# Kernel tuning notes

Measured on AMD Instinct MI355X. Metric: run time of the kernel, lower is better.

The kernel has to match this reference:

```python
import jax, jax.numpy as jnp
import numpy as np

E, D, H = 8, 512, 2048  # num_experts, features, features*mlp_ratio
B, S = 4, 512


def _lecun(key, shape):
    fan_in = shape[-2] if len(shape) >= 2 else shape[0]
    return jax.random.normal(key, shape, dtype=jnp.float32) / jnp.sqrt(jnp.float32(fan_in))


def setup_inputs() -> dict:
    key = jax.random.key(0)
    ks = jax.random.split(key, 8)
    return {
        'x_real': jax.random.normal(ks[0], (B, S, D), dtype=jnp.float32),
        'x_imag': jax.random.normal(ks[1], (B, S, D), dtype=jnp.float32),
        # gating Dense over concat([amp, phase]) -> in_features = 2*D
        'gate_W': _lecun(ks[2], (2 * D, E)),
        'gate_b': jnp.zeros((E,), jnp.float32),
        # per-expert ComplexLinear 1: D -> H
        'W1r': _lecun(ks[3], (E, D, H)),
        'W1i': _lecun(ks[4], (E, D, H)),
        'b1r': jnp.zeros((E, H), jnp.float32),
        'b1i': jnp.zeros((E, H), jnp.float32),
        # per-expert ComplexModReLU bias
        'mod_b': jnp.zeros((E, H), jnp.float32),
        # per-expert ComplexLinear 2: H -> D
        'W2r': _lecun(ks[5], (E, H, D)),
        'W2i': _lecun(ks[6], (E, H, D)),
        'b2r': jnp.zeros((E, D), jnp.float32),
        'b2i': jnp.zeros((E, D), jnp.float32),
    }


def reference(x_real, x_imag, gate_W, gate_b, W1r, W1i, b1r, b1i, mod_b, W2r, W2i, b2r, b2i):
    eps = 1e-10
    # --- gating: scores over [|z|, angle(z)] ---
    amp = jnp.sqrt(x_real ** 2 + x_imag ** 2)            # |z|, [B,S,D]
    phase = jnp.arctan2(x_imag, x_real)                  # angle(z)
    routing_input = jnp.concatenate([amp, phase], axis=-1)  # [B,S,2D]
    scores = routing_input @ gate_W + gate_b             # [B,S,E]
    probs = jax.nn.softmax(scores, axis=-1)
    idx = jnp.argmax(probs, axis=-1)                     # [B,S] top-1 expert

    # --- all experts dense (faithful to reference): complex linear 1 ---
    # (Wr + iWi)(xr + ixi) : hr = xr Wr - xi Wi ; hi = xr Wi + xi Wr
    h_r = (jnp.einsum('bsd,edh->ebsh', x_real, W1r)
           - jnp.einsum('bsd,edh->ebsh', x_imag, W1i)) + b1r[:, None, None, :]
    h_i = (jnp.einsum('bsd,edh->ebsh', x_real, W1i)
           + jnp.einsum('bsd,edh->ebsh', x_imag, W1r)) + b1i[:, None, None, :]

    # --- ComplexModReLU: relu(|z|+b) * z / (|z|+eps), |z| = sqrt(r^2+i^2+eps) ---
    a = jnp.sqrt(h_r ** 2 + h_i ** 2 + eps)              # [E,B,S,H]
    scale = jax.nn.relu(a + mod_b[:, None, None, :]) / (a + eps)
    h_r = h_r * scale
    h_i = h_i * scale

    # --- complex linear 2 ---
    o_r = (jnp.einsum('ebsh,ehd->ebsd', h_r, W2r)
           - jnp.einsum('ebsh,ehd->ebsd', h_i, W2i)) + b2r[:, None, None, :]
    o_i = (jnp.einsum('ebsh,ehd->ebsd', h_r, W2i)
           + jnp.einsum('ebsh,ehd->ebsd', h_i, W2r)) + b2i[:, None, None, :]

    # --- mask + weight (top-1): out = sum_e out_e * probs[...,e] * (argmax==e) ---
    e_ids = jnp.arange(probs.shape[-1])
    w = jnp.transpose(probs, (2, 0, 1)) * (idx[None, :, :] == e_ids[:, None, None])  # [E,B,S]
    out_r = jnp.einsum('ebs,ebsd->bsd', w, o_r)
    out_i = jnp.einsum('ebs,ebsd->bsd', w, o_i)
    return (out_r, out_i)
```

## Files before the change

### kernel.cpp

```cpp
#include <hip/hip_runtime.h>
#include <math.h>

#define NE 8
#define ND 512
#define NH 2048
#define NT 2048

typedef __attribute__((ext_vector_type(8)))  short short8;
typedef __attribute__((ext_vector_type(16))) float f32x16;

#define GLL(g, d) __builtin_amdgcn_global_load_lds( \
    (const __attribute__((address_space(1))) void*)(g), \
    (__attribute__((address_space(3))) void*)(d), 16, 0, 0)

__device__ __forceinline__ unsigned short f2bf(float x) {
    unsigned int u = __builtin_bit_cast(unsigned int, x);
    u += 0x7FFFu + ((u >> 16) & 1u);
    return (unsigned short)(u >> 16);
}

__device__ __forceinline__ short8 neg8(short8 v) {
    int4 u = __builtin_bit_cast(int4, v);
    u.x ^= 0x80008000; u.y ^= 0x80008000; u.z ^= 0x80008000; u.w ^= 0x80008000;
    return __builtin_bit_cast(short8, u);
}

__device__ __forceinline__ short8 lds8(const unsigned short* p) {
    return *(const short8*)p;
}

__global__ __launch_bounds__(256) void gate_kernel(
    const float* __restrict__ xr, const float* __restrict__ xi,
    const float* __restrict__ gW, const float* __restrict__ gb,
    float* __restrict__ gate_w,
    int* __restrict__ counts, int* __restrict__ tok_list,
    unsigned short* __restrict__ xbr, unsigned short* __restrict__ xbi)
{
    int t = blockIdx.x;
    int tid = threadIdx.x;
    const float* xrt = xr + (size_t)t * ND;
    const float* xit = xi + (size_t)t * ND;
    unsigned short* obr = xbr + (size_t)t * ND;
    unsigned short* obi = xbi + (size_t)t * ND;

    float acc[NE] = {0,0,0,0,0,0,0,0};
    for (int r = tid; r < 2 * ND; r += 256) {
        int d = r & (ND - 1);
        float a = xrt[d], b = xit[d];
        float v;
        if (r < ND) {
            v = sqrtf(a * a + b * b);
            obr[d] = f2bf(a);
            obi[d] = f2bf(b);
        } else {
            v = atan2f(b, a);
        }
        const float4* g = (const float4*)(gW + (size_t)r * NE);
        float4 g0 = g[0], g1 = g[1];
        acc[0] += v * g0.x; acc[1] += v * g0.y; acc[2] += v * g0.z; acc[3] += v * g0.w;
        acc[4] += v * g1.x; acc[5] += v * g1.y; acc[6] += v * g1.z; acc[7] += v * g1.w;
    }
    #pragma unroll
    for (int e = 0; e < NE; e++) {
        for (int off = 32; off > 0; off >>= 1)
            acc[e] += __shfl_down(acc[e], off, 64);
    }
    __shared__ float part[4][NE];
    int wave = tid >> 6, lane = tid & 63;
    if (lane == 0) {
        #pragma unroll
        for (int e = 0; e < NE; e++) part[wave][e] = acc[e];
    }
    __syncthreads();
    if (tid == 0) {
        float s[NE];
        #pragma unroll
        for (int e = 0; e < NE; e++)
            s[e] = part[0][e] + part[1][e] + part[2][e] + part[3][e] + gb[e];
        int amax = 0; float m = s[0];
        #pragma unroll
        for (int e = 1; e < NE; e++) if (s[e] > m) { m = s[e]; amax = e; }
        float denom = 0.f;
        #pragma unroll
        for (int e = 0; e < NE; e++) denom += expf(s[e] - m);
        gate_w[t] = 1.0f / denom;
        int pos = atomicAdd(&counts[amax], 1);
        tok_list[amax * NT + pos] = t;
    }
}

__global__ __launch_bounds__(256) void transw_kernel(
    const float* __restrict__ s0, unsigned short* __restrict__ d0,
    const float* __restrict__ s1, unsigned short* __restrict__ d1,
    int R, int C)
{
    __shared__ unsigned int tile[64 * 33];
    int e = blockIdx.z;
    int c0 = blockIdx.x * 64, r0 = blockIdx.y * 64;
    size_t off = (size_t)e * R * C;
    int tid = threadIdx.x;
    int rl = tid >> 4;
    int c4 = (tid & 15) * 4;
    int r4 = (tid & 15) * 4;
    #pragma unroll
    for (int p = 0; p < 2; ++p) {
        const float* src = (p ? s1 : s0) + off;
        unsigned short* dst = (p ? d1 : d0) + off;
        if (p) __syncthreads();
        #pragma unroll
        for (int jj = 0; jj < 4; ++jj) {
            int r = rl + 16 * jj;
            float4 v = *(const float4*)(src + (size_t)(r0 + r) * C + c0 + c4);
            tile[r * 33 + (c4 >> 1)]     = ((unsigned)f2bf(v.y) << 16) | f2bf(v.x);
            tile[r * 33 + (c4 >> 1) + 1] = ((unsigned)f2bf(v.w) << 16) | f2bf(v.z);
        }
        __syncthreads();
        #pragma unroll
        for (int ii = 0; ii < 4; ++ii) {
            int c = (tid >> 4) + 16 * ii;
            unsigned short o[4];
            #pragma unroll
            for (int j = 0; j < 4; ++j) {
                unsigned int u = tile[(r4 + j) * 33 + (c >> 1)];
                o[j] = (c & 1) ? (unsigned short)(u >> 16) : (unsigned short)(u & 0xFFFF);
            }
            *(ushort4*)(dst + (size_t)(c0 + c) * R + r0 + r4) = make_ushort4(o[0], o[1], o[2], o[3]);
        }
        if (p == 0) __syncthreads();
    }
}

__global__ __launch_bounds__(256, 3) void moe1_kernel(
    const unsigned short* __restrict__ xbr, const unsigned short* __restrict__ xbi,
    const unsigned short* __restrict__ w1tr, const unsigned short* __restrict__ w1ti,
    const float* __restrict__ b1r, const float* __restrict__ b1i,
    const float* __restrict__ mod_b,
    const int* __restrict__ counts, const int* __restrict__ tok_list,
    unsigned short* __restrict__ hr, unsigned short* __restrict__ hi)
{
    int e = blockIdx.z;
    int n = counts[e];
    int mbase = blockIdx.y * 64;
    if (mbase >= n) return;
    int n0 = blockIdx.x * 128;
    int tid = threadIdx.x;
    int w = tid >> 6, l = tid & 63;
    int l31 = l & 31, half = l >> 5;
    int mw = w & 1, nw = w >> 1;

    __shared__ unsigned short sAr[64 * 64];
    __shared__ unsigned short sAi[64 * 64];
    __shared__ unsigned short sBr[128 * 64];
    __shared__ unsigned short sBi[128 * 64];
    __shared__ int toks[64];

    const int* tl = tok_list + e * NT;
    if (tid < 64) {
        int idx = mbase + tid;
        toks[tid] = tl[idx < n ? idx : n - 1];
    }
    __syncthreads();

    int c8 = tid & 7;
    int rloc = tid >> 3;
    int gc8 = (c8 ^ (rloc & 7)) * 8;
    int tA0 = toks[rloc], tA1 = toks[rloc + 32];
    const unsigned short* gAr0 = xbr + (size_t)tA0 * ND + gc8;
    const unsigned short* gAi0 = xbi + (size_t)tA0 * ND + gc8;
    const unsigned short* gAr1 = xbr + (size_t)tA1 * ND + gc8;
    const unsigned short* gAi1 = xbi + (size_t)tA1 * ND + gc8;
    size_t brow = (size_t)e * NH + n0 + rloc;
    const unsigned short* gBr0 = w1tr + (brow +  0) * ND + gc8;
    const unsigned short* gBr1 = w1tr + (brow + 32) * ND + gc8;
    const unsigned short* gBr2 = w1tr + (brow + 64) * ND + gc8;
    const unsigned short* gBr3 = w1tr + (brow + 96) * ND + gc8;
    const unsigned short* gBi0 = w1ti + (brow +  0) * ND + gc8;
    const unsigned short* gBi1 = w1ti + (brow + 32) * ND + gc8;
    const unsigned short* gBi2 = w1ti + (brow + 64) * ND + gc8;
    const unsigned short* gBi3 = w1ti + (brow + 96) * ND + gc8;

    int dA = rloc * 64 + c8 * 8;
    unsigned short* dAr0 = sAr + dA;          unsigned short* dAr1 = sAr + dA + 32 * 64;
    unsigned short* dAi0 = sAi + dA;          unsigned short* dAi1 = sAi + dA + 32 * 64;
    unsigned short* dBr0 = sBr + dA;          unsigned short* dBr1 = sBr + dA + 32 * 64;
    unsigned short* dBr2 = sBr + dA + 64*64;  unsigned short* dBr3 = sBr + dA + 96 * 64;
    unsigned short* dBi0 = sBi + dA;          unsigned short* dBi1 = sBi + dA + 32 * 64;
    unsigned short* dBi2 = sBi + dA + 64*64;  unsigned short* dBi3 = sBi + dA + 96 * 64;

    f32x16 accr[2] = {}, acci[2] = {};
    int am = mw * 32 + l31;
    int aoffBase = am * 64;
    int bn0 = nw * 64 + l31;
    int bn1 = nw * 64 + 32 + l31;

    for (int kt = 0; kt < ND / 64; ++kt) {
        __syncthreads();
        int ko = kt * 64;
        GLL(gAr0 + ko, dAr0); GLL(gAr1 + ko, dAr1);
        GLL(gAi0 + ko, dAi0); GLL(gAi1 + ko, dAi1);
        GLL(gBr0 + ko, dBr0); GLL(gBr1 + ko, dBr1);
        GLL(gBr2 + ko, dBr2); GLL(gBr3 + ko, dBr3);
        GLL(gBi0 + ko, dBi0); GLL(gBi1 + ko, dBi1);
        GLL(gBi2 + ko, dBi2); GLL(gBi3 + ko, dBi3);
        __syncthreads();
        #pragma unroll
        for (int ks = 0; ks < 4; ++ks) {
            int kc = ks * 2 + half;
            int ao = aoffBase + ((kc ^ (am & 7)) * 8);
            short8 ar = lds8(sAr + ao);
            short8 ai = lds8(sAi + ao);
            short8 an = neg8(ai);
            int bo0 = bn0 * 64 + ((kc ^ (bn0 & 7)) * 8);
            int bo1 = bn1 * 64 + ((kc ^ (bn1 & 7)) * 8);
            short8 br0 = lds8(sBr + bo0), bi0 = lds8(sBi + bo0);
            short8 br1 = lds8(sBr + bo1), bi1 = lds8(sBi + bo1);
            accr[0] = __builtin_amdgcn_mfma_f32_32x32x16_bf16(ar, br0, accr[0], 0, 0, 0);
            accr[0] = __builtin_amdgcn_mfma_f32_32x32x16_bf16(an, bi0, accr[0], 0, 0, 0);
            acci[0] = __builtin_amdgcn_mfma_f32_32x32x16_bf16(ar, bi0, acci[0], 0, 0, 0);
            acci[0] = __builtin_amdgcn_mfma_f32_32x32x16_bf16(ai, br0, acci[0], 0, 0, 0);
            accr[1] = __builtin_amdgcn_mfma_f32_32x32x16_bf16(ar, br1, accr[1], 0, 0, 0);
            accr[1] = __builtin_amdgcn_mfma_f32_32x32x16_bf16(an, bi1, accr[1], 0, 0, 0);
            acci[1] = __builtin_amdgcn_mfma_f32_32x32x16_bf16(ar, bi1, acci[1], 0, 0, 0);
            acci[1] = __builtin_amdgcn_mfma_f32_32x32x16_bf16(ai, br1, acci[1], 0, 0, 0);
        }
    }

    #pragma unroll
    for (int ns = 0; ns < 2; ++ns) {
        int col = n0 + nw * 64 + ns * 32 + l31;
        float bre = b1r[(size_t)e * NH + col];
        float bie = b1i[(size_t)e * NH + col];
        float mbv = mod_b[(size_t)e * NH + col];
        #pragma unroll
        for (int reg = 0; reg < 16; ++reg) {
            int row = (reg & 3) + 8 * (reg >> 2) + 4 * half;
            int tix = mw * 32 + row;
            if (mbase + tix >= n) continue;
            int tok = toks[tix];
            float vr = accr[ns][reg] + bre;
            float vi = acci[ns][reg] + bie;
            float a = sqrtf(vr * vr + vi * vi + 1e-10f);
            float sc = fmaxf(a + mbv, 0.0f) / (a + 1e-10f);
            hr[(size_t)tok * NH + col] = f2bf(vr * sc);
            hi[(size_t)tok * NH + col] = f2bf(vi * sc);
        }
    }
}

__global__ __launch_bounds__(256, 4) void moe2_kernel(
    const unsigned short* __restrict__ hr, const unsigned short* __restrict__ hi,
    const unsigned short* __restrict__ w2tr, const unsigned short* __restrict__ w2ti,
    const float* __restrict__ b2r, const float* __restrict__ b2i,
    const int* __restrict__ counts, const int* __restrict__ tok_list,
    const float* __restrict__ gate_w,
    float* __restrict__ out)
{
    int e = blockIdx.z >> 2;
    int ksl = blockIdx.z & 3;
    int n = counts[e];
    int mbase = blockIdx.y * 64;
    if (mbase >= n) return;
    int n0 = blockIdx.x * 64;
    int kbase = ksl * (NH / 4);
    int tid = threadIdx.x;
    int w = tid >> 6, l = tid & 63;
    int l31 = l & 31, half = l >> 5;
    int mw = w & 1, nw = w >> 1;

    __shared__ unsigned short sAr[64 * 64];
    __shared__ unsigned short sAi[64 * 64];
    __shared__ unsigned short sBr[64 * 64];
    __shared__ unsigned short sBi[64 * 64];
    __shared__ int toks[64];

    const int* tl = tok_list + e * NT;
    if (tid < 64) {
        int idx = mbase + tid;
        toks[tid] = tl[idx < n ? idx : n - 1];
    }
    __syncthreads();

    int c8 = tid & 7;
    int rloc = tid >> 3;
    int gc8 = (c8 ^ (rloc & 7)) * 8;
    int tA0 = toks[rloc], tA1 = toks[rloc + 32];
    const unsigned short* gAr0 = hr + (size_t)tA0 * NH + kbase + gc8;
    const unsigned short* gAi0 = hi + (size_t)tA0 * NH + kbase + gc8;
    const unsigned short* gAr1 = hr + (size_t)tA1 * NH + kbase + gc8;
    const unsigned short* gAi1 = hi + (size_t)tA1 * NH + kbase + gc8;
    size_t brow = (size_t)e * ND + n0 + rloc;
    const unsigned short* gBr0 = w2tr + (brow +  0) * NH + kbase + gc8;
    const unsigned short* gBr1 = w2tr + (brow + 32) * NH + kbase + gc8;
    const unsigned short* gBi0 = w2ti + (brow +  0) * NH + kbase + gc8;
    const unsigned short* gBi1 = w2ti + (brow + 32) * NH + kbase + gc8;

    int dA = rloc * 64 + c8 * 8;
    unsigned short* dAr0 = sAr + dA; unsigned short* dAr1 = sAr + dA + 32 * 64;
    unsigned short* dAi0 = sAi + dA; unsigned short* dAi1 = sAi + dA + 32 * 64;
    unsigned short* dBr0 = sBr + dA; unsigned short* dBr1 = sBr + dA + 32 * 64;
    unsigned short* dBi0 = sBi + dA; unsigned short* dBi1 = sBi + dA + 32 * 64;

    f32x16 accr = {}, acci = {};
    int am = mw * 32 + l31;
    int aoffBase = am * 64;
    int bn = nw * 32 + l31;
    int boffBase = bn * 64;

    for (int kt = 0; kt < (NH / 4) / 64; ++kt) {
        __syncthreads();
        int ko = kt * 64;
        GLL(gAr0 + ko, dAr0); GLL(gAr1 + ko, dAr1);
        GLL(gAi0 + ko, dAi0); GLL(gAi1 + ko, dAi1);
        GLL(gBr0 + ko, dBr0); GLL(gBr1 + ko, dBr1);
        GLL(gBi0 + ko, dBi0); GLL(gBi1 + ko, dBi1);
        __syncthreads();
        #pragma unroll
        for (int ks = 0; ks < 4; ++ks) {
            int kc = ks * 2 + half;
            int ao = aoffBase + ((kc ^ (am & 7)) * 8);
            short8 ar = lds8(sAr + ao);
            short8 ai = lds8(sAi + ao);
            short8 an = neg8(ai);
            int bo = boffBase + ((kc ^ (bn & 7)) * 8);
            short8 br = lds8(sBr + bo), bi = lds8(sBi + bo);
            accr = __builtin_amdgcn_mfma_f32_32x32x16_bf16(ar, br, accr, 0, 0, 0);
            accr = __builtin_amdgcn_mfma_f32_32x32x16_bf16(an, bi, accr, 0, 0, 0);
            acci = __builtin_amdgcn_mfma_f32_32x32x16_bf16(ar, bi, acci, 0, 0, 0);
            acci = __builtin_amdgcn_mfma_f32_32x32x16_bf16(ai, br, acci, 0, 0, 0);
        }
    }

    int col = n0 + nw * 32 + l31;
    float bre = (ksl == 0) ? b2r[(size_t)e * ND + col] : 0.0f;
    float bie = (ksl == 0) ? b2i[(size_t)e * ND + col] : 0.0f;
    #pragma unroll
    for (int reg = 0; reg < 16; ++reg) {
        int row = (reg & 3) + 8 * (reg >> 2) + 4 * half;
        int tix = mw * 32 + row;
        if (mbase + tix >= n) continue;
        int tok = toks[tix];
        float gw = gate_w[tok];
        atomicAdd(&out[(size_t)tok * ND + col], (accr[reg] + bre) * gw);
        atomicAdd(&out[(size_t)NT * ND + (size_t)tok * ND + col], (acci[reg] + bie) * gw);
    }
}

extern "C" void kernel_launch(void* const* d_in, const int* in_sizes, int n_in,
                              void* d_out, int out_size, void* d_ws, size_t ws_size,
                              hipStream_t stream) {
    const float* xr   = (const float*)d_in[0];
    const float* xi   = (const float*)d_in[1];
    const float* gW   = (const float*)d_in[2];
    const float* gb   = (const float*)d_in[3];
    const float* W1r  = (const float*)d_in[4];
    const float* W1i  = (const float*)d_in[5];
    const float* b1r  = (const float*)d_in[6];
    const float* b1i  = (const float*)d_in[7];
    const float* modb = (const float*)d_in[8];
    const float* W2r  = (const float*)d_in[9];
    const float* W2i  = (const float*)d_in[10];
    const float* b2r  = (const float*)d_in[11];
    const float* b2i  = (const float*)d_in[12];
    float* out = (float*)d_out;

    char* ws = (char*)d_ws;
    int*   counts   = (int*)ws;
    float* gate_w   = (float*)(ws + 256);
    int*   tok_list = (int*)(ws + 256 + 8192);
    size_t off = 256 + 8192 + (size_t)NE * NT * 4;
    unsigned short* xbr  = (unsigned short*)(ws + off); off += (size_t)NT * ND * 2;
    unsigned short* xbi  = (unsigned short*)(ws + off); off += (size_t)NT * ND * 2;
    unsigned short* w1tr = (unsigned short*)(ws + off); off += (size_t)NE * ND * NH * 2;
    unsigned short* w1ti = (unsigned short*)(ws + off); off += (size_t)NE * ND * NH * 2;
    unsigned short* w2tr = (unsigned short*)(ws + off); off += (size_t)NE * ND * NH * 2;
    unsigned short* w2ti = (unsigned short*)(ws + off); off += (size_t)NE * ND * NH * 2;
    unsigned short* h_r  = (unsigned short*)(ws + off); off += (size_t)NT * NH * 2;
    unsigned short* h_i  = (unsigned short*)(ws + off); off += (size_t)NT * NH * 2;

    hipMemsetAsync(counts, 0, 64 * sizeof(int), stream);
    hipMemsetAsync(out, 0, (size_t)out_size * sizeof(float), stream);
    gate_kernel<<<NT, 256, 0, stream>>>(xr, xi, gW, gb, gate_w, counts, tok_list, xbr, xbi);
    transw_kernel<<<dim3(NH / 64, ND / 64, NE), 256, 0, stream>>>(W1r, w1tr, W1i, w1ti, ND, NH);
    transw_kernel<<<dim3(ND / 64, NH / 64, NE), 256, 0, stream>>>(W2r, w2tr, W2i, w2ti, NH, ND);
    moe1_kernel<<<dim3(NH / 128, NT / 64, NE), 256, 0, stream>>>(
        xbr, xbi, w1tr, w1ti, b1r, b1i, modb, counts, tok_list, h_r, h_i);
    moe2_kernel<<<dim3(ND / 64, NT / 64, NE * 4), 256, 0, stream>>>(
        h_r, h_i, w2tr, w2ti, b2r, b2i, counts, tok_list, gate_w, out);
}
```

Before: 318.2 us.

## Stage token rows once in LDS and stream expert weights directly from global

Both MoE GEMM kernels now copy the whole K-extent of the gathered activation rows (32 tokens) into LDS once. Weight fragments are read straight from global memory into registers each k-step instead of being staged through LDS in 64-wide k-tiles with two barriers per tile. Tiles change to 32 tokens by 256 output columns, with each wave owning 64 columns, and occupancy hints drop to 2. This removes the per-k-step barrier and LDS traffic for the weights. In exchange, the strided global weight loads sit on the MFMA critical path without software prefetch, and each weight byte is reused across fewer tokens per block.

```diff
diff --git a/kernel.cpp b/kernel.cpp
--- a/kernel.cpp
+++ b/kernel.cpp
@@ -26,6 +26,9 @@
 }
 
 __device__ __forceinline__ short8 lds8(const unsigned short* p) {
+    return *(const short8*)p;
+}
+__device__ __forceinline__ short8 glb8(const unsigned short* p) {
     return *(const short8*)p;
 }
 
@@ -130,7 +133,7 @@
     }
 }
 
-__global__ __launch_bounds__(256, 3) void moe1_kernel(
+__global__ __launch_bounds__(256, 2) void moe1_kernel(
     const unsigned short* __restrict__ xbr, const unsigned short* __restrict__ xbi,
     const unsigned short* __restrict__ w1tr, const unsigned short* __restrict__ w1ti,
     const float* __restrict__ b1r, const float* __restrict__ b1i,
@@ -140,105 +143,81 @@
 {
     int e = blockIdx.z;
     int n = counts[e];
-    int mbase = blockIdx.y * 64;
+    int mbase = blockIdx.y * 32;
     if (mbase >= n) return;
-    int n0 = blockIdx.x * 128;
+    int n0 = blockIdx.x * 256;
     int tid = threadIdx.x;
     int w = tid >> 6, l = tid & 63;
     int l31 = l & 31, half = l >> 5;
-    int mw = w & 1, nw = w >> 1;
-
-    __shared__ unsigned short sAr[64 * 64];
-    __shared__ unsigned short sAi[64 * 64];
-    __shared__ unsigned short sBr[128 * 64];
-    __shared__ unsigned short sBi[128 * 64];
-    __shared__ int toks[64];
+
+    __shared__ unsigned short sAr[32 * 512];
+    __shared__ unsigned short sAi[32 * 512];
+    __shared__ int toks[32];
 
     const int* tl = tok_list + e * NT;
-    if (tid < 64) {
+    if (tid < 32) {
         int idx = mbase + tid;
         toks[tid] = tl[idx < n ? idx : n - 1];
     }
     __syncthreads();
 
-    int c8 = tid & 7;
-    int rloc = tid >> 3;
-    int gc8 = (c8 ^ (rloc & 7)) * 8;
-    int tA0 = toks[rloc], tA1 = toks[rloc + 32];
-    const unsigned short* gAr0 = xbr + (size_t)tA0 * ND + gc8;
-    const unsigned short* gAi0 = xbi + (size_t)tA0 * ND + gc8;
-    const unsigned short* gAr1 = xbr + (size_t)tA1 * ND + gc8;
-    const unsigned short* gAi1 = xbi + (size_t)tA1 * ND + gc8;
-    size_t brow = (size_t)e * NH + n0 + rloc;
-    const unsigned short* gBr0 = w1tr + (brow +  0) * ND + gc8;
-    const unsigned short* gBr1 = w1tr + (brow + 32) * ND + gc8;
-    const unsigned short* gBr2 = w1tr + (brow + 64) * ND + gc8;
-    const unsigned short* gBr3 = w1tr + (brow + 96) * ND + gc8;
-    const unsigned short* gBi0 = w1ti + (brow +  0) * ND + gc8;
-    const unsigned short* gBi1 = w1ti + (brow + 32) * ND + gc8;
-    const unsigned short* gBi2 = w1ti + (brow + 64) * ND + gc8;
-    const unsigned short* gBi3 = w1ti + (brow + 96) * ND + gc8;
-
-    int dA = rloc * 64 + c8 * 8;
-    unsigned short* dAr0 = sAr + dA;          unsigned short* dAr1 = sAr + dA + 32 * 64;
-    unsigned short* dAi0 = sAi + dA;          unsigned short* dAi1 = sAi + dA + 32 * 64;
-    unsigned short* dBr0 = sBr + dA;          unsigned short* dBr1 = sBr + dA + 32 * 64;
-    unsigned short* dBr2 = sBr + dA + 64*64;  unsigned short* dBr3 = sBr + dA + 96 * 64;
-    unsigned short* dBi0 = sBi + dA;          unsigned short* dBi1 = sBi + dA + 32 * 64;
-    unsigned short* dBi2 = sBi + dA + 64*64;  unsigned short* dBi3 = sBi + dA + 96 * 64;
-
-    f32x16 accr[2] = {}, acci[2] = {};
-    int am = mw * 32 + l31;
-    int aoffBase = am * 64;
-    int bn0 = nw * 64 + l31;
-    int bn1 = nw * 64 + 32 + l31;
-
-    for (int kt = 0; kt < ND / 64; ++kt) {
-        __syncthreads();
-        int ko = kt * 64;
-        GLL(gAr0 + ko, dAr0); GLL(gAr1 + ko, dAr1);
-        GLL(gAi0 + ko, dAi0); GLL(gAi1 + ko, dAi1);
-        GLL(gBr0 + ko, dBr0); GLL(gBr1 + ko, dBr1);
-        GLL(gBr2 + ko, dBr2); GLL(gBr3 + ko, dBr3);
-        GLL(gBi0 + ko, dBi0); GLL(gBi1 + ko, dBi1);
-        GLL(gBi2 + ko, dBi2); GLL(gBi3 + ko, dBi3);
-        __syncthreads();
-        #pragma unroll
-        for (int ks = 0; ks < 4; ++ks) {
-            int kc = ks * 2 + half;
-            int ao = aoffBase + ((kc ^ (am & 7)) * 8);
-            short8 ar = lds8(sAr + ao);
-            short8 ai = lds8(sAi + ao);
-            short8 an = neg8(ai);
-            int bo0 = bn0 * 64 + ((kc ^ (bn0 & 7)) * 8);
-            int bo1 = bn1 * 64 + ((kc ^ (bn1 & 7)) * 8);
-            short8 br0 = lds8(sBr + bo0), bi0 = lds8(sBi + bo0);
-            short8 br1 = lds8(sBr + bo1), bi1 = lds8(sBi + bo1);
-            accr[0] = __builtin_amdgcn_mfma_f32_32x32x16_bf16(ar, br0, accr[0], 0, 0, 0);
-            accr[0] = __builtin_amdgcn_mfma_f32_32x32x16_bf16(an, bi0, accr[0], 0, 0, 0);
-            acci[0] = __builtin_amdgcn_mfma_f32_32x32x16_bf16(ar, bi0, acci[0], 0, 0, 0);
-            acci[0] = __builtin_amdgcn_mfma_f32_32x32x16_bf16(ai, br0, acci[0], 0, 0, 0);
-            accr[1] = __builtin_amdgcn_mfma_f32_32x32x16_bf16(ar, br1, accr[1], 0, 0, 0);
-            accr[1] = __builtin_amdgcn_mfma_f32_32x32x16_bf16(an, bi1, accr[1], 0, 0, 0);
-            acci[1] = __builtin_amdgcn_mfma_f32_32x32x16_bf16(ar, bi1, acci[1], 0, 0, 0);
-            acci[1] = __builtin_amdgcn_mfma_f32_32x32x16_bf16(ai, br1, acci[1], 0, 0, 0);
-        }
+    #pragma unroll
+    for (int j = 0; j < 8; ++j) {
+        int row = w * 8 + j;
+        int tok = toks[row];
+        int src = (l ^ (row & 7)) * 8;
+        GLL(xbr + (size_t)tok * ND + src, &sAr[row * 512]);
+        GLL(xbi + (size_t)tok * ND + src, &sAi[row * 512]);
+    }
+    __syncthreads();
+
+    size_t bbase = ((size_t)e * NH + n0 + w * 64 + l31) * ND + half * 8;
+    const unsigned short* pBr0 = w1tr + bbase;
+    const unsigned short* pBi0 = w1ti + bbase;
+    const unsigned short* pBr1 = w1tr + bbase + (size_t)32 * ND;
+    const unsigned short* pBi1 = w1ti + bbase + (size_t)32 * ND;
+
+    int arow = l31 * 512;
+    int axor = l31 & 7;
+
+    f32x16 accr0 = {}, acci0 = {}, accr1 = {}, acci1 = {};
+
+    #pragma unroll 4
+    for (int ks = 0; ks < 32; ++ks) {
+        int kc = ks * 2 + half;
+        int ao = arow + ((kc ^ axor) * 8);
+        short8 ar = lds8(sAr + ao);
+        short8 ai = lds8(sAi + ao);
+        short8 an = neg8(ai);
+        short8 br0 = glb8(pBr0 + ks * 16);
+        short8 bi0 = glb8(pBi0 + ks * 16);
+        short8 br1 = glb8(pBr1 + ks * 16);
+        short8 bi1 = glb8(pBi1 + ks * 16);
+        accr0 = __builtin_amdgcn_mfma_f32_32x32x16_bf16(ar, br0, accr0, 0, 0, 0);
+        accr0 = __builtin_amdgcn_mfma_f32_32x32x16_bf16(an, bi0, accr0, 0, 0, 0);
+        acci0 = __builtin_amdgcn_mfma_f32_32x32x16_bf16(ar, bi0, acci0, 0, 0, 0);
+        acci0 = __builtin_amdgcn_mfma_f32_32x32x16_bf16(ai, br0, acci0, 0, 0, 0);
+        accr1 = __builtin_amdgcn_mfma_f32_32x32x16_bf16(ar, br1, accr1, 0, 0, 0);
+        accr1 = __builtin_amdgcn_mfma_f32_32x32x16_bf16(an, bi1, accr1, 0, 0, 0);
+        acci1 = __builtin_amdgcn_mfma_f32_32x32x16_bf16(ar, bi1, acci1, 0, 0, 0);
+        acci1 = __builtin_amdgcn_mfma_f32_32x32x16_bf16(ai, br1, acci1, 0, 0, 0);
     }
 
     #pragma unroll
     for (int ns = 0; ns < 2; ++ns) {
-        int col = n0 + nw * 64 + ns * 32 + l31;
+        int col = n0 + w * 64 + ns * 32 + l31;
         float bre = b1r[(size_t)e * NH + col];
         float bie = b1i[(size_t)e * NH + col];
         float mbv = mod_b[(size_t)e * NH + col];
+        const f32x16& cr = ns ? accr1 : accr0;
+        const f32x16& ci = ns ? acci1 : acci0;
         #pragma unroll
         for (int reg = 0; reg < 16; ++reg) {
             int row = (reg & 3) + 8 * (reg >> 2) + 4 * half;
-            int tix = mw * 32 + row;
-            if (mbase + tix >= n) continue;
-            int tok = toks[tix];
-            float vr = accr[ns][reg] + bre;
-            float vi = acci[ns][reg] + bie;
+            if (mbase + row >= n) continue;
+            int tok = toks[row];
+            float vr = cr[reg] + bre;
+            float vi = ci[reg] + bie;
             float a = sqrtf(vr * vr + vi * vi + 1e-10f);
             float sc = fmaxf(a + mbv, 0.0f) / (a + 1e-10f);
             hr[(size_t)tok * NH + col] = f2bf(vr * sc);
@@ -247,7 +226,7 @@
     }
 }
 
-__global__ __launch_bounds__(256, 4) void moe2_kernel(
+__global__ __launch_bounds__(256, 2) void moe2_kernel(
     const unsigned short* __restrict__ hr, const unsigned short* __restrict__ hi,
     const unsigned short* __restrict__ w2tr, const unsigned short* __restrict__ w2ti,
     const float* __restrict__ b2r, const float* __restrict__ b2i,
@@ -258,90 +237,83 @@
     int e = blockIdx.z >> 2;
     int ksl = blockIdx.z & 3;
     int n = counts[e];
-    int mbase = blockIdx.y * 64;
+    int mbase = blockIdx.y * 32;
     if (mbase >= n) return;
-    int n0 = blockIdx.x * 64;
+    int n0 = blockIdx.x * 256;
     int kbase = ksl * (NH / 4);
     int tid = threadIdx.x;
     int w = tid >> 6, l = tid & 63;
     int l31 = l & 31, half = l >> 5;
-    int mw = w & 1, nw = w >> 1;
-
-    __shared__ unsigned short sAr[64 * 64];
-    __shared__ unsigned short sAi[64 * 64];
-    __shared__ unsigned short sBr[64 * 64];
-    __shared__ unsigned short sBi[64 * 64];
-    __shared__ int toks[64];
+
+    __shared__ unsigned short sAr[32 * 512];
+    __shared__ unsigned short sAi[32 * 512];
+    __shared__ int toks[32];
 
     const int* tl = tok_list + e * NT;
-    if (tid < 64) {
+    if (tid < 32) {
         int idx = mbase + tid;
         toks[tid] = tl[idx < n ? idx : n - 1];
     }
     __syncthreads();
 
-    int c8 = tid & 7;
-    int rloc = tid >> 3;
-    int gc8 = (c8 ^ (rloc & 7)) * 8;
-    int tA0 = toks[rloc], tA1 = toks[rloc + 32];
-    const unsigned short* gAr0 = hr + (size_t)tA0 * NH + kbase + gc8;
-    const unsigned short* gAi0 = hi + (size_t)tA0 * NH + kbase + gc8;
-    const unsigned short* gAr1 = hr + (size_t)tA1 * NH + kbase + gc8;
-    const unsigned short* gAi1 = hi + (size_t)tA1 * NH + kbase + gc8;
-    size_t brow = (size_t)e * ND + n0 + rloc;
-    const unsigned short* gBr0 = w2tr + (brow +  0) * NH + kbase + gc8;
-    const unsigned short* gBr1 = w2tr + (brow + 32) * NH + kbase + gc8;
-    const unsigned short* gBi0 = w2ti + (brow +  0) * NH + kbase + gc8;
-    const unsigned short* gBi1 = w2ti + (brow + 32) * NH + kbase + gc8;
-
-    int dA = rloc * 64 + c8 * 8;
-    unsigned short* dAr0 = sAr + dA; unsigned short* dAr1 = sAr + dA + 32 * 64;
-    unsigned short* dAi0 = sAi + dA; unsigned short* dAi1 = sAi + dA + 32 * 64;
-    unsigned short* dBr0 = sBr + dA; unsigned short* dBr1 = sBr + dA + 32 * 64;
-    unsigned short* dBi0 = sBi + dA; unsigned short* dBi1 = sBi + dA + 32 * 64;
-
-    f32x16 accr = {}, acci = {};
-    int am = mw * 32 + l31;
-    int aoffBase = am * 64;
-    int bn = nw * 32 + l31;
-    int boffBase = bn * 64;
-
-    for (int kt = 0; kt < (NH / 4) / 64; ++kt) {
-        __syncthreads();
-        int ko = kt * 64;
-        GLL(gAr0 + ko, dAr0); GLL(gAr1 + ko, dAr1);
-        GLL(gAi0 + ko, dAi0); GLL(gAi1 + ko, dAi1);
-        GLL(gBr0 + ko, dBr0); GLL(gBr1 + ko, dBr1);
-        GLL(gBi0 + ko, dBi0); GLL(gBi1 + ko, dBi1);
-        __syncthreads();
-        #pragma unroll
-        for (int ks = 0; ks < 4; ++ks) {
-            int kc = ks * 2 + half;
-            int ao = aoffBase + ((kc ^ (am & 7)) * 8);
-            short8 ar = lds8(sAr + ao);
-            short8 ai = lds8(sAi + ao);
-            short8 an = neg8(ai);
-            int bo = boffBase + ((kc ^ (bn & 7)) * 8);
-            short8 br = lds8(sBr + bo), bi = lds8(sBi + bo);
-            accr = __builtin_amdgcn_mfma_f32_32x32x16_bf16(ar, br, accr, 0, 0, 0);
-            accr = __builtin_amdgcn_mfma_f32_32x32x16_bf16(an, bi, accr, 0, 0, 0);
-            acci = __builtin_amdgcn_mfma_f32_32x32x16_bf16(ar, bi, acci, 0, 0, 0);
-            acci = __builtin_amdgcn_mfma_f32_32x32x16_bf16(ai, br, acci, 0, 0, 0);
-        }
-    }
-
-    int col = n0 + nw * 32 + l31;
-    float bre = (ksl == 0) ? b2r[(size_t)e * ND + col] : 0.0f;
-    float bie = (ksl == 0) ? b2i[(size_t)e * ND + col] : 0.0f;
-    #pragma unroll
-    for (int reg = 0; reg < 16; ++reg) {
-        int row = (reg & 3) + 8 * (reg >> 2) + 4 * half;
-        int tix = mw * 32 + row;
-        if (mbase + tix >= n) continue;
-        int tok = toks[tix];
-        float gw = gate_w[tok];
-        atomicAdd(&out[(size_t)tok * ND + col], (accr[reg] + bre) * gw);
-        atomicAdd(&out[(size_t)NT * ND + (size_t)tok * ND + col], (acci[reg] + bie) * gw);
+    #pragma unroll
+    for (int j = 0; j < 8; ++j) {
+        int row = w * 8 + j;
+        int tok = toks[row];
+        int src = (l ^ (row & 7)) * 8;
+        GLL(hr + (size_t)tok * NH + kbase + src, &sAr[row * 512]);
+        GLL(hi + (size_t)tok * NH + kbase + src, &sAi[row * 512]);
+    }
+    __syncthreads();
+
+    size_t bbase = ((size_t)e * ND + n0 + w * 64 + l31) * NH + kbase + half * 8;
+    const unsigned short* pBr0 = w2tr + bbase;
+    const unsigned short* pBi0 = w2ti + bbase;
+    const unsigned short* pBr1 = w2tr + bbase + (size_t)32 * NH;
+    const unsigned short* pBi1 = w2ti + bbase + (size_t)32 * NH;
+
+    int arow = l31 * 512;
+    int axor = l31 & 7;
+
+    f32x16 accr0 = {}, acci0 = {}, accr1 = {}, acci1 = {};
+
+    #pragma unroll 4
+    for (int ks = 0; ks < 32; ++ks) {
+        int kc = ks * 2 + half;
+        int ao = arow + ((kc ^ axor) * 8);
+        short8 ar = lds8(sAr + ao);
+        short8 ai = lds8(sAi + ao);
+        short8 an = neg8(ai);
+        short8 br0 = glb8(pBr0 + ks * 16);
+        short8 bi0 = glb8(pBi0 + ks * 16);
+        short8 br1 = glb8(pBr1 + ks * 16);
+        short8 bi1 = glb8(pBi1 + ks * 16);
+        accr0 = __builtin_amdgcn_mfma_f32_32x32x16_bf16(ar, br0, accr0, 0, 0, 0);
+        accr0 = __builtin_amdgcn_mfma_f32_32x32x16_bf16(an, bi0, accr0, 0, 0, 0);
+        acci0 = __builtin_amdgcn_mfma_f32_32x32x16_bf16(ar, bi0, acci0, 0, 0, 0);
+        acci0 = __builtin_amdgcn_mfma_f32_32x32x16_bf16(ai, br0, acci0, 0, 0, 0);
+        accr1 = __builtin_amdgcn_mfma_f32_32x32x16_bf16(ar, br1, accr1, 0, 0, 0);
+        accr1 = __builtin_amdgcn_mfma_f32_32x32x16_bf16(an, bi1, accr1, 0, 0, 0);
+        acci1 = __builtin_amdgcn_mfma_f32_32x32x16_bf16(ar, bi1, acci1, 0, 0, 0);
+        acci1 = __builtin_amdgcn_mfma_f32_32x32x16_bf16(ai, br1, acci1, 0, 0, 0);
+    }
+
+    #pragma unroll
+    for (int ns = 0; ns < 2; ++ns) {
+        int col = n0 + w * 64 + ns * 32 + l31;
+        float bre = (ksl == 0) ? b2r[(size_t)e * ND + col] : 0.0f;
+        float bie = (ksl == 0) ? b2i[(size_t)e * ND + col] : 0.0f;
+        const f32x16& cr = ns ? accr1 : accr0;
+        const f32x16& ci = ns ? acci1 : acci0;
+        #pragma unroll
+        for (int reg = 0; reg < 16; ++reg) {
+            int row = (reg & 3) + 8 * (reg >> 2) + 4 * half;
+            if (mbase + row >= n) continue;
+            int tok = toks[row];
+            float gw = gate_w[tok];
+            atomicAdd(&out[(size_t)tok * ND + col], (cr[reg] + bre) * gw);
+            atomicAdd(&out[(size_t)NT * ND + (size_t)tok * ND + col], (ci[reg] + bie) * gw);
+        }
     }
 }
 
@@ -382,8 +354,8 @@
     gate_kernel<<<NT, 256, 0, stream>>>(xr, xi, gW, gb, gate_w, counts, tok_list, xbr, xbi);
     transw_kernel<<<dim3(NH / 64, ND / 64, NE), 256, 0, stream>>>(W1r, w1tr, W1i, w1ti, ND, NH);
     transw_kernel<<<dim3(ND / 64, NH / 64, NE), 256, 0, stream>>>(W2r, w2tr, W2i, w2ti, NH, ND);
-    moe1_kernel<<<dim3(NH / 128, NT / 64, NE), 256, 0, stream>>>(
+    moe1_kernel<<<dim3(NH / 256, NT / 32, NE), 256, 0, stream>>>(
         xbr, xbi, w1tr, w1ti, b1r, b1i, modb, counts, tok_list, h_r, h_i);
-    moe2_kernel<<<dim3(ND / 64, NT / 64, NE * 4), 256, 0, stream>>>(
+    moe2_kernel<<<dim3(ND / 256, NT / 32, NE * 4), 256, 0, stream>>>(
         h_r, h_i, w2tr, w2ti, b2r, b2i, counts, tok_list, gate_w, out);
 }
```

Result: slower. 454.5 us (+42.8%).
